# Kernel optimization log

Measured on AMD Instinct MI355X. Metric: run time of the kernel, lower is better.

The kernel has to match this reference:

```python
import jax, jax.numpy as jnp
import numpy as np

N, D, C, P = 4096, 512, 100, 64
EPS_COS = 1e-8   # torch cosine_similarity norm clamp
EPS_INV = 1e-5   # module's 1/(d + 1e-5)


def setup_inputs() -> dict:
    key = jax.random.key(0)
    k1, k2, k3, k4 = jax.random.split(key, 4)
    feats = jax.random.normal(k1, (N, D), dtype=jnp.float32)
    protos = jax.random.normal(k2, (C, P, D), dtype=jnp.float32)
    cls_ids = jax.random.randint(k3, (N,), 0, C)
    proto_labels = jax.random.randint(k4, (C, P), 0, 1000)
    return {"feats": feats, "protos": protos, "cls_ids": cls_ids,
            "proto_labels": proto_labels}


def reference(feats, protos, cls_ids, proto_labels):
    # Gather each box's class-conditional prototype set: [N, P, D]
    p = protos[cls_ids]
    pl = proto_labels[cls_ids]                       # [N, P]

    # cosine distance: 1 - f.p / (max(|f|,eps) * max(|p|,eps))
    dot = jnp.einsum('nd,npd->np', feats, p)         # [N, P]
    fnorm = jnp.maximum(jnp.linalg.norm(feats, axis=-1, keepdims=True), EPS_COS)
    pnorm = jnp.maximum(jnp.linalg.norm(p, axis=-1), EPS_COS)
    d_cos = 1.0 - dot / (fnorm * pnorm)

    diff = feats[:, None, :] - p                     # [N, P, D]
    d_l1 = jnp.mean(jnp.abs(diff), axis=-1)          # F.l1_loss (mean)
    d_l2 = jnp.mean(diff * diff, axis=-1)            # F.mse_loss (mean)

    dists = jnp.stack([d_cos, d_l1, d_l2], axis=1)   # [N, 3, P]
    probs = jax.nn.softmax(1.0 / (dists + EPS_INV), axis=-1).mean(axis=1)  # [N, P]

    idx = jnp.argmax(probs, axis=-1)                 # [N]
    labels = jnp.take_along_axis(pl, idx[:, None], axis=1)[:, 0]
    return labels, probs
```

## Files before the change

kernel.cpp:

```cpp
#include <hip/hip_runtime.h>

#define D 512
#define P 64
#define CHUNK 4
#define MAXD 1536
#define EPS_COS 1e-8f
#define EPS_INV 1e-5f


__device__ __forceinline__ float wave_sum(float v) {
#pragma unroll
    for (int m = 32; m >= 1; m >>= 1) v += __shfl_xor(v, m, 64);
    return v;
}

__global__ __launch_bounds__(256) void prep_kernel(
    const float* __restrict__ protos, const int* __restrict__ cls,
    float* __restrict__ pp, int* __restrict__ sorted, int* __restrict__ desc,
    int N, int C, int rows)
{
    if (blockIdx.x != 0) {
        const int lane = threadIdx.x & 63;
        const int r = (blockIdx.x - 1) * 4 + (threadIdx.x >> 6);
        if (r >= rows) return;
        const float* row = protos + (size_t)r * D;
        const float4 a = *(const float4*)(row + lane * 4);
        const float4 b = *(const float4*)(row + 256 + lane * 4);
        float s = a.x*a.x + a.y*a.y + a.z*a.z + a.w*a.w
                + b.x*b.x + b.y*b.y + b.z*b.z + b.w*b.w;
        s = wave_sum(s);
        if (lane == 0) pp[r] = s;
        return;
    }

    __shared__ int cnt[128], fl[128], exc[128], arr[128];
    const int t = threadIdx.x;
    if (t < 128) { cnt[t] = 0; fl[t] = 0; arr[t] = 0; }
    for (int i = t; i < 3 * MAXD; i += 256) desc[i] = 0;
    __syncthreads();
#pragma unroll
    for (int k = 0; k < 16; ++k) {
        const int n = t + 256 * k;
        if (n < N) atomicAdd(&cnt[cls[n]], 1);
    }
    __syncthreads();
    int v = 0, gv = 0, pos = 0;
    if (t < 128) {
        v = cnt[t];
        gv = (v + CHUNK - 1) / CHUNK;
        pos = ((t & 7) << 4) | (t >> 3);
        exc[t] = v;
        arr[pos] = gv;
    }
    __syncthreads();
    for (int d = 1; d < 128; d <<= 1) {
        int a = 0, b = 0;
        if (t < 128 && t >= d) { a = exc[t - d]; b = arr[t - d]; }
        __syncthreads();
        if (t < 128 && t >= d) { exc[t] += a; arr[t] += b; }
        __syncthreads();
    }
    const int base = (t < 128) ? exc[t] - v : 0;
    __syncthreads();
    if (t < 128) exc[t] = base;
    __syncthreads();
    if (t < C && gv > 0) {
        const int bucket = t & 7;
        const int bstart = bucket ? arr[(bucket << 4) - 1] : 0;
        const int localoff = (arr[pos] - gv) - bstart;
        for (int k = 0; k < gv; ++k) {
            const int slot = ((localoff + k) << 3) | bucket;
            if (slot < MAXD) {
                desc[3*slot+0] = t;
                desc[3*slot+1] = base + CHUNK * k;
                desc[3*slot+2] = min(CHUNK, v - CHUNK * k);
            }
        }
    }
#pragma unroll
    for (int k = 0; k < 16; ++k) {
        const int n = t + 256 * k;
        if (n < N) {
            const int c = cls[n];
            const int p2 = exc[c] + atomicAdd(&fl[c], 1);
            sorted[p2] = n;
        }
    }
}

__global__ __launch_bounds__(128) void proto_main_kernel(
    const float* __restrict__ feats,
    const float* __restrict__ protos,
    const int*   __restrict__ proto_labels,
    const float* __restrict__ ppbuf,
    const int*   __restrict__ sorted,
    const int*   __restrict__ desc,
    float* __restrict__ out, int N)
{
    const int di  = blockIdx.x;
    const int cnt = desc[3*di+2];
    if (cnt == 0) return;
    const int cls   = desc[3*di+0];
    const int start = desc[3*di+1];
    const int lane = threadIdx.x & 63;
    const int wave = threadIdx.x >> 6;

    int  nidx[2];
    bool valid[2];
#pragma unroll
    for (int k = 0; k < 2; ++k) {
        const int pos = wave + 2 * k;
        valid[k] = pos < cnt;
        nidx[k]  = sorted[start + (valid[k] ? pos : (cnt - 1))];
    }

    float4 f0[2], f1[2];
    float  ff[2];
#pragma unroll
    for (int b = 0; b < 2; ++b) {
        const float* f = feats + (size_t)nidx[b] * D;
        f0[b] = *(const float4*)(f + lane * 4);
        f1[b] = *(const float4*)(f + 256 + lane * 4);
        float s = f0[b].x*f0[b].x + f0[b].y*f0[b].y + f0[b].z*f0[b].z + f0[b].w*f0[b].w
                + f1[b].x*f1[b].x + f1[b].y*f1[b].y + f1[b].z*f1[b].z + f1[b].w*f1[b].w;
        ff[b] = wave_sum(s);
    }

    const float* pr = protos + (size_t)cls * (P * D);
    const int jsel = (lane >> 3) & 7;
    const int gown = lane & 7;
    const bool hi32 = (lane & 32) != 0;
    const bool hi16 = (lane & 16) != 0;
    const bool hi8  = (lane & 8)  != 0;

    float r_dot[2] = {0.f, 0.f}, r_l1[2] = {0.f, 0.f};

    for (int g = 0; g < 8; ++g) {
        float pd[2][8], pl[2][8];
#pragma unroll
        for (int j = 0; j < 8; ++j) {
            const float* row = pr + (size_t)(8 * g + j) * D;
            const float4 q0 = *(const float4*)(row + lane * 4);
            const float4 q1 = *(const float4*)(row + 256 + lane * 4);
#pragma unroll
            for (int b = 0; b < 2; ++b) {
                float dot, l1, t;
                dot  = f0[b].x*q0.x; t = f0[b].x - q0.x; l1  = fabsf(t);
                dot += f0[b].y*q0.y; t = f0[b].y - q0.y; l1 += fabsf(t);
                dot += f0[b].z*q0.z; t = f0[b].z - q0.z; l1 += fabsf(t);
                dot += f0[b].w*q0.w; t = f0[b].w - q0.w; l1 += fabsf(t);
                dot += f1[b].x*q1.x; t = f1[b].x - q1.x; l1 += fabsf(t);
                dot += f1[b].y*q1.y; t = f1[b].y - q1.y; l1 += fabsf(t);
                dot += f1[b].z*q1.z; t = f1[b].z - q1.z; l1 += fabsf(t);
                dot += f1[b].w*q1.w; t = f1[b].w - q1.w; l1 += fabsf(t);
                pd[b][j] = dot; pl[b][j] = l1;
            }
        }
#pragma unroll
        for (int b = 0; b < 2; ++b) {
#pragma unroll
            for (int k = 0; k < 4; ++k) {
                const float sd = hi32 ? pd[b][k] : pd[b][k+4];
                const float sl = hi32 ? pl[b][k] : pl[b][k+4];
                const float rd = __shfl_xor(sd, 32, 64);
                const float rl = __shfl_xor(sl, 32, 64);
                pd[b][k] = (hi32 ? pd[b][k+4] : pd[b][k]) + rd;
                pl[b][k] = (hi32 ? pl[b][k+4] : pl[b][k]) + rl;
            }
#pragma unroll
            for (int k = 0; k < 2; ++k) {
                const float sd = hi16 ? pd[b][k] : pd[b][k+2];
                const float sl = hi16 ? pl[b][k] : pl[b][k+2];
                const float rd = __shfl_xor(sd, 16, 64);
                const float rl = __shfl_xor(sl, 16, 64);
                pd[b][k] = (hi16 ? pd[b][k+2] : pd[b][k]) + rd;
                pl[b][k] = (hi16 ? pl[b][k+2] : pl[b][k]) + rl;
            }
            {
                const float sd = hi8 ? pd[b][0] : pd[b][1];
                const float sl = hi8 ? pl[b][0] : pl[b][1];
                const float rd = __shfl_xor(sd, 8, 64);
                const float rl = __shfl_xor(sl, 8, 64);
                pd[b][0] = (hi8 ? pd[b][1] : pd[b][0]) + rd;
                pl[b][0] = (hi8 ? pl[b][1] : pl[b][0]) + rl;
            }
#pragma unroll
            for (int m = 4; m >= 1; m >>= 1) {
                pd[b][0] += __shfl_xor(pd[b][0], m, 64);
                pl[b][0] += __shfl_xor(pl[b][0], m, 64);
            }
            if (gown == g) { r_dot[b] = pd[b][0]; r_l1[b] = pl[b][0]; }
        }
    }

    const int myp = 8 * gown + jsel;
    const float s_pp  = ppbuf[cls * P + myp];
    const float pnorm = fmaxf(sqrtf(s_pp), EPS_COS);

#pragma unroll
    for (int b = 0; b < 2; ++b) {
        const float fnorm = fmaxf(sqrtf(ff[b]), EPS_COS);
        const float d_cos = 1.0f - r_dot[b] / (fnorm * pnorm);
        const float d_l1  = r_l1[b] * (1.0f / (float)D);
        const float d_l2  = (ff[b] - 2.0f * r_dot[b] + s_pp) * (1.0f / (float)D);

        float sc[3];
        sc[0] = 1.0f / (d_cos + EPS_INV);
        sc[1] = 1.0f / (d_l1  + EPS_INV);
        sc[2] = 1.0f / (d_l2  + EPS_INV);

        float prob = 0.f;
#pragma unroll
        for (int i = 0; i < 3; ++i) {
            float m = sc[i];
#pragma unroll
            for (int w = 32; w >= 1; w >>= 1) m = fmaxf(m, __shfl_xor(m, w, 64));
            const float e = expf(sc[i] - m);
            prob += e / wave_sum(e);
        }
        prob *= (1.0f / 3.0f);

        float best = prob;
        int   bidx = myp;
#pragma unroll
        for (int w = 32; w >= 1; w >>= 1) {
            const float ov = __shfl_xor(best, w, 64);
            const int   oi = __shfl_xor(bidx, w, 64);
            if (ov > best || (ov == best && oi < bidx)) { best = ov; bidx = oi; }
        }

        if (valid[b]) {
            out[(size_t)N + (size_t)nidx[b] * P + myp] = prob;
            if (lane == 0) out[nidx[b]] = (float)proto_labels[cls * P + bidx];
        }
    }
}

extern "C" void kernel_launch(void* const* d_in, const int* in_sizes, int n_in,
                              void* d_out, int out_size, void* d_ws, size_t ws_size,
                              hipStream_t stream) {
    const float* feats        = (const float*)d_in[0];
    const float* protos       = (const float*)d_in[1];
    const int*   cls_ids      = (const int*)d_in[2];
    const int*   proto_labels = (const int*)d_in[3];
    float* out = (float*)d_out;

    const int N    = in_sizes[2];
    const int rows = in_sizes[1] / D;
    const int C    = rows / P;

    char* w = (char*)d_ws;
    float* pp     = (float*)w;
    int*   sorted = (int*)(w + 25600);
    int*   desc   = (int*)(w + 41984);

    prep_kernel<<<1 + (rows + 3) / 4, 256, 0, stream>>>(
        protos, cls_ids, pp, sorted, desc, N, C, rows);
    proto_main_kernel<<<MAXD, 128, 0, stream>>>(
        feats, protos, proto_labels, pp, sorted, desc, out, N);
}
```

Measured before the change: 114.2 us.

## Split prototype set across wave pairs and gather distances through shared memory

The main kernel goes from 128 to 256 threads per block. Each pair of waves now splits the 64 prototypes in half, so each wave handles 32 prototypes for two feature rows instead of 64. Partial dot and L1 results go to shared memory, and after a barrier each wave runs the softmax/argmax epilogue for one row, with one lane per prototype. This halves the serial per-wave loop and adds parallelism, at the cost of feature loads duplicated across the pair, an LDS round trip and a block-wide sync.

```diff
diff --git a/kernel.cpp b/kernel.cpp
--- a/kernel.cpp
+++ b/kernel.cpp
@@ -88,7 +88,7 @@
     }
 }
 
-__global__ __launch_bounds__(128) void proto_main_kernel(
+__global__ __launch_bounds__(256, 4) void proto_main_kernel(
     const float* __restrict__ feats,
     const float* __restrict__ protos,
     const int*   __restrict__ proto_labels,
@@ -97,6 +97,9 @@
     const int*   __restrict__ desc,
     float* __restrict__ out, int N)
 {
+    __shared__ float dist[CHUNK * P * 2];
+    __shared__ float ffbuf[CHUNK];
+
     const int di  = blockIdx.x;
     const int cnt = desc[3*di+2];
     if (cnt == 0) return;
@@ -104,38 +107,41 @@
     const int start = desc[3*di+1];
     const int lane = threadIdx.x & 63;
     const int wave = threadIdx.x >> 6;
-
-    int  nidx[2];
-    bool valid[2];
+    const int pair = wave >> 1;
+    const int h    = wave & 1;
+
+    int nidx[2];
 #pragma unroll
     for (int k = 0; k < 2; ++k) {
-        const int pos = wave + 2 * k;
-        valid[k] = pos < cnt;
-        nidx[k]  = sorted[start + (valid[k] ? pos : (cnt - 1))];
+        const int pos = 2 * pair + k;
+        nidx[k] = sorted[start + (pos < cnt ? pos : cnt - 1)];
     }
 
     float4 f0[2], f1[2];
-    float  ff[2];
 #pragma unroll
     for (int b = 0; b < 2; ++b) {
         const float* f = feats + (size_t)nidx[b] * D;
         f0[b] = *(const float4*)(f + lane * 4);
         f1[b] = *(const float4*)(f + 256 + lane * 4);
-        float s = f0[b].x*f0[b].x + f0[b].y*f0[b].y + f0[b].z*f0[b].z + f0[b].w*f0[b].w
-                + f1[b].x*f1[b].x + f1[b].y*f1[b].y + f1[b].z*f1[b].z + f1[b].w*f1[b].w;
-        ff[b] = wave_sum(s);
-    }
-
-    const float* pr = protos + (size_t)cls * (P * D);
-    const int jsel = (lane >> 3) & 7;
-    const int gown = lane & 7;
+    }
+    if (h == 0) {
+        float s0 = f0[0].x*f0[0].x + f0[0].y*f0[0].y + f0[0].z*f0[0].z + f0[0].w*f0[0].w
+                 + f1[0].x*f1[0].x + f1[0].y*f1[0].y + f1[0].z*f1[0].z + f1[0].w*f1[0].w;
+        float s1 = f0[1].x*f0[1].x + f0[1].y*f0[1].y + f0[1].z*f0[1].z + f0[1].w*f0[1].w
+                 + f1[1].x*f1[1].x + f1[1].y*f1[1].y + f1[1].z*f1[1].z + f1[1].w*f1[1].w;
+        s0 = wave_sum(s0);
+        s1 = wave_sum(s1);
+        if (lane == 0) { ffbuf[2*pair] = s0; ffbuf[2*pair+1] = s1; }
+    }
+
+    const float* pr = protos + (size_t)cls * (P * D) + (size_t)(32 * h) * D;
     const bool hi32 = (lane & 32) != 0;
     const bool hi16 = (lane & 16) != 0;
     const bool hi8  = (lane & 8)  != 0;
 
-    float r_dot[2] = {0.f, 0.f}, r_l1[2] = {0.f, 0.f};
-
-    for (int g = 0; g < 8; ++g) {
+    float r_dot[2], r_l1[2];
+
+    for (int g = 0; g < 4; ++g) {
         float pd[2][8], pl[2][8];
 #pragma unroll
         for (int j = 0; j < 8; ++j) {
@@ -189,20 +195,31 @@
                 pd[b][0] += __shfl_xor(pd[b][0], m, 64);
                 pl[b][0] += __shfl_xor(pl[b][0], m, 64);
             }
-            if (gown == g) { r_dot[b] = pd[b][0]; r_l1[b] = pl[b][0]; }
-        }
-    }
-
-    const int myp = 8 * gown + jsel;
-    const float s_pp  = ppbuf[cls * P + myp];
-    const float pnorm = fmaxf(sqrtf(s_pp), EPS_COS);
-
-#pragma unroll
-    for (int b = 0; b < 2; ++b) {
-        const float fnorm = fmaxf(sqrtf(ff[b]), EPS_COS);
-        const float d_cos = 1.0f - r_dot[b] / (fnorm * pnorm);
-        const float d_l1  = r_l1[b] * (1.0f / (float)D);
-        const float d_l2  = (ff[b] - 2.0f * r_dot[b] + s_pp) * (1.0f / (float)D);
+            if ((lane & 3) == g) { r_dot[b] = pd[b][0]; r_l1[b] = pl[b][0]; }
+        }
+    }
+
+    {
+        const int pg   = 32 * h + 8 * (lane & 3) + ((lane >> 3) & 7);
+        const int qsel = (lane >> 2) & 1;
+#pragma unroll
+        for (int k = 0; k < 2; ++k) {
+            dist[((2 * pair + k) * P + pg) * 2 + qsel] = qsel ? r_l1[k] : r_dot[k];
+        }
+    }
+    __syncthreads();
+
+    const int s = wave;
+    if (s < cnt) {
+        const int n = sorted[start + s];
+        const float2 dl = *(const float2*)&dist[(s * P + lane) * 2];
+        const float ffv   = ffbuf[s];
+        const float ppv   = ppbuf[cls * P + lane];
+        const float fnorm = fmaxf(sqrtf(ffv), EPS_COS);
+        const float pnorm = fmaxf(sqrtf(ppv), EPS_COS);
+        const float d_cos = 1.0f - dl.x / (fnorm * pnorm);
+        const float d_l1  = dl.y * (1.0f / (float)D);
+        const float d_l2  = (ffv - 2.0f * dl.x + ppv) * (1.0f / (float)D);
 
         float sc[3];
         sc[0] = 1.0f / (d_cos + EPS_INV);
@@ -221,7 +238,7 @@
         prob *= (1.0f / 3.0f);
 
         float best = prob;
-        int   bidx = myp;
+        int   bidx = lane;
 #pragma unroll
         for (int w = 32; w >= 1; w >>= 1) {
             const float ov = __shfl_xor(best, w, 64);
@@ -229,10 +246,8 @@
             if (ov > best || (ov == best && oi < bidx)) { best = ov; bidx = oi; }
         }
 
-        if (valid[b]) {
-            out[(size_t)N + (size_t)nidx[b] * P + myp] = prob;
-            if (lane == 0) out[nidx[b]] = (float)proto_labels[cls * P + bidx];
-        }
+        out[(size_t)N + (size_t)n * P + lane] = prob;
+        if (lane == 0) out[n] = (float)proto_labels[cls * P + bidx];
     }
 }
 
@@ -256,6 +271,6 @@
 
     prep_kernel<<<1 + (rows + 3) / 4, 256, 0, stream>>>(
         protos, cls_ids, pp, sorted, desc, N, C, rows);
-    proto_main_kernel<<<MAXD, 128, 0, stream>>>(
+    proto_main_kernel<<<MAXD, 256, 0, stream>>>(
         feats, protos, proto_labels, pp, sorted, desc, out, N);
 }
```

Result: no change. 113.0 us (-1.0%).
